# Performance work log

Hardware: AMD Instinct MI355X
Metric: run time of the kernel (lower is better)

## Reference

```python
import jax, jax.numpy as jnp
import numpy as np

NU, NI, ED, H = 30000, 10000, 64, 4
D = ED * H            # fusion_dim = 256
N = NU + NI           # total graph nodes
E = 100000            # edges
B = 8192              # scored (user, wine) pairs
NST, SD = 4, 64       # side tokens / side token dim
NEG = -1e30


def setup_inputs():
    key = jax.random.key(0)
    ks = iter(jax.random.split(key, 64))

    def w(*shape):
        return jax.random.normal(next(ks), shape, jnp.float32) * 0.05

    return {
        "user": jax.random.randint(next(ks), (B,), 0, NU),
        "wine": jax.random.randint(next(ks), (B,), 0, NI),
        "edge_index": jax.random.randint(next(ks), (2, E), 0, N),
        "keep_edge": jax.random.uniform(next(ks), (E,)) > 0.2,   # edge_dropout keep mask
        "node_mask": jax.random.uniform(next(ks), (N,)) < 0.2,   # mask-autoencoding mask
        "user_emb": w(NU, ED),
        "wine_emb": w(NI, ED),
        "up_w": w(ED, D), "up_b": w(D),
        "wp_w": w(ED, D), "wp_b": w(D),
        "sf_proj_w": w(SD, D), "sf_proj_b": w(D),
        "sf_q_w": w(D, D), "sf_q_b": w(D),
        "sf_k_w": w(D, D), "sf_k_b": w(D),
        "sf_v_w": w(D, D), "sf_v_b": w(D),
        "sf_o_w": w(D, D), "sf_o_b": w(D),
        "sf_fc_w": w(2 * D, D), "sf_fc_b": w(D),
        "g_w": w(D, D), "g_b": w(D),
        "t_q_w": w(D, H * D), "t_q_b": w(H * D),
        "t_k_w": w(D, H * D), "t_k_b": w(H * D),
        "t_v_w": w(D, H * D), "t_v_b": w(H * D),
        "t_skip_w": w(D, D), "t_skip_b": w(D),
        "fc_w": w(2 * D, 1), "fc_b": w(1),
        "ae_w": w(D, D), "ae_b": w(D),
        "ep_w": w(2 * D, 1), "ep_b": w(1),
        "wine_side_features": jax.random.normal(next(ks), (NI, NST, SD), jnp.float32),
    }


def _forward(user, wine, edge_index, keep_edge, node_mask,
             user_emb, wine_emb, up_w, up_b, wp_w, wp_b,
             sf_proj_w, sf_proj_b, sf_q_w, sf_q_b, sf_k_w, sf_k_b,
             sf_v_w, sf_v_b, sf_o_w, sf_o_b, sf_fc_w, sf_fc_b,
             g_w, g_b, t_q_w, t_q_b, t_k_w, t_k_b, t_v_w, t_v_b,
             t_skip_w, t_skip_b, fc_w, fc_b, ae_w, ae_b, ep_w, ep_b,
             wine_side_features):
    u_proj = user_emb @ up_w + up_b                       # [NU, D]
    w_proj = wine_emb @ wp_w + wp_b                       # [NI, D]

    # WineSideFusion: single-head attention of wine embedding over side tokens
    side = wine_side_features @ sf_proj_w + sf_proj_b     # [NI, T, D]
    q = w_proj @ sf_q_w + sf_q_b                          # [NI, D]
    k = side @ sf_k_w + sf_k_b                            # [NI, T, D]
    v = side @ sf_v_w + sf_v_b
    attn = jax.nn.softmax(jnp.einsum('nd,ntd->nt', q, k) / jnp.sqrt(jnp.float32(D)), axis=-1)
    ao = jnp.einsum('nt,ntd->nd', attn, v) @ sf_o_w + sf_o_b
    fused = jnp.concatenate([w_proj, ao], axis=1) @ sf_fc_w + sf_fc_b

    x = jnp.concatenate([u_proj, fused], axis=0)          # [N, D]
    src, dst = edge_index[0], edge_index[1]
    ew = keep_edge.astype(x.dtype)                        # edge dropout as 0/1 weights

    # GCNConv (add self loops, symmetric norm)
    deg = jax.ops.segment_sum(ew, dst, num_segments=N) + 1.0
    dinv = jax.lax.rsqrt(deg)
    norm = dinv[src] * dinv[dst] * ew                     # [E]
    xw = x @ g_w                                          # [N, D]
    agg = jax.ops.segment_sum(xw[src] * norm[:, None], dst, num_segments=N)
    x = agg + xw * (dinv * dinv)[:, None] + g_b

    # TransformerConv(heads=H, concat=False): mean over heads + skip
    qh = (x @ t_q_w + t_q_b).reshape(N, H, D)
    kh = (x @ t_k_w + t_k_b).reshape(N, H, D)
    vh = (x @ t_v_w + t_v_b).reshape(N, H, D)
    logits = jnp.einsum('ehd,ehd->eh', qh[dst], kh[src]) / jnp.sqrt(jnp.float32(D))
    logits = jnp.where(keep_edge[:, None], logits, NEG)
    m = jax.ops.segment_max(logits, dst, num_segments=N)  # [N, H]
    m = jnp.where(m < NEG / 2, 0.0, m)                    # guard empty segments
    e = jnp.exp(logits - m[dst]) * ew[:, None]            # [E, H]
    den = jax.ops.segment_sum(e, dst, num_segments=N)     # [N, H]
    num = jax.ops.segment_sum(e[:, :, None] * vh[src], dst, num_segments=N)  # [N, H, D]
    attn_out = num / jnp.maximum(den, 1e-16)[:, :, None]
    x = attn_out.mean(axis=1) + x @ t_skip_w + t_skip_b   # [N, D]

    # Masked autoencoding: masked rows are zeroed, then autoencoded -> recon = bias
    maskf = node_mask.astype(x.dtype)
    recon = ae_b                                          # 0 @ ae_w + ae_b
    diff = recon[None, :] - x                             # [N, D]
    recon_loss = jnp.sum(maskf[:, None] * diff * diff) / (jnp.sum(maskf) * D)

    u_out = x[user]                                       # [B, D]
    w_out = x[wine + NU]                                  # [B, D]
    pair = jnp.concatenate([u_out, w_out], axis=1)        # [B, 2D]

    edge_score = jax.nn.sigmoid(pair @ ep_w + ep_b)       # [B, 1]
    edge_pred_loss = jnp.mean((edge_score - 1.0) ** 2)

    score = jax.nn.sigmoid((pair @ fc_w + fc_b).squeeze(-1)) * 4.0 + 1.0  # [B]
    return score, recon_loss, edge_pred_loss


def reference(user, wine, edge_index, keep_edge, node_mask,
              user_emb, wine_emb, up_w, up_b, wp_w, wp_b,
              sf_proj_w, sf_proj_b, sf_q_w, sf_q_b, sf_k_w, sf_k_b,
              sf_v_w, sf_v_b, sf_o_w, sf_o_b, sf_fc_w, sf_fc_b,
              g_w, g_b, t_q_w, t_q_b, t_k_w, t_k_b, t_v_w, t_v_b,
              t_skip_w, t_skip_b, fc_w, fc_b, ae_w, ae_b, ep_w, ep_b,
              wine_side_features):
    return _forward(user, wine, edge_index, keep_edge, node_mask,
                    user_emb, wine_emb, up_w, up_b, wp_w, wp_b,
                    sf_proj_w, sf_proj_b, sf_q_w, sf_q_b, sf_k_w, sf_k_b,
                    sf_v_w, sf_v_b, sf_o_w, sf_o_b, sf_fc_w, sf_fc_b,
                    g_w, g_b, t_q_w, t_q_b, t_k_w, t_k_b, t_v_w, t_v_b,
                    t_skip_w, t_skip_b, fc_w, fc_b, ae_w, ae_b, ep_w, ep_b,
                    wine_side_features)
```

## Files before the change

### kernel.cpp

```cpp
#include <hip/hip_runtime.h>
#include <stdint.h>

typedef unsigned short u16;
typedef unsigned char u8;
typedef __attribute__((ext_vector_type(8))) short bf16x8;
typedef __attribute__((ext_vector_type(4))) float f32x4;

#define NU_C 30000
#define NI_C 10000
#define N_C  40000
#define E_C  100000
#define B_C  8192

static __device__ __forceinline__ float bf2f(u16 u) {
    union { unsigned int i; float f; } c; c.i = ((unsigned int)u) << 16; return c.f;
}
static __device__ __forceinline__ u16 f2bf(float f) {
    union { float f; unsigned int i; } c; c.f = f;
    return (u16)((c.i + 0x7FFFu + ((c.i >> 16) & 1u)) >> 16);
}
static __device__ __forceinline__ float wave_sum(float v) {
#pragma unroll
    for (int off = 32; off > 0; off >>= 1) v += __shfl_xor(v, off);
    return v;
}

__global__ void zero_kernel(unsigned int* p, int n) {
    int i = blockIdx.x * 256 + threadIdx.x;
    if (i < n) p[i] = 0u;
}
__global__ void fillval_kernel(float* p, int n, float v) {
    int i = blockIdx.x * 256 + threadIdx.x;
    if (i < n) p[i] = v;
}

__global__ void detect_kernel(const unsigned int* a, int n, int* flag) {
    int i = blockIdx.x * 256 + threadIdx.x;
    if (i >= n) return;
    unsigned int v = a[i];
    int f = 0;
    if (v > 1u) f |= 1;
    if (v != 0u && v != 0x3F800000u) f |= 2;
    if (f) atomicOr(flag, f);
}
__global__ void conv_masks_kernel(const void* keep_raw, const void* nm_raw,
                                  u8* km, u8* nm, int E, int N, const int* flag)
{
    int i = blockIdx.x * 256 + threadIdx.x;
    const int f = *flag;
    if (i < E) {
        u8 r;
        if ((f & 1) == 0)      r = ((const int*)keep_raw)[i] != 0;
        else if ((f & 2) == 0) r = ((const float*)keep_raw)[i] != 0.f;
        else                   r = ((const u8*)keep_raw)[i] != 0;
        km[i] = r;
    }
    int j = i - E;
    if (j >= 0 && j < N) {
        u8 r;
        if ((f & 1) == 0)      r = ((const int*)nm_raw)[j] != 0;
        else if ((f & 2) == 0) r = ((const float*)nm_raw)[j] != 0.f;
        else                   r = ((const u8*)nm_raw)[j] != 0;
        nm[j] = r;
    }
}

__global__ void conv3_kernel(const float* __restrict__ a, int na4,
                             const float* __restrict__ b, int nb4,
                             const float* __restrict__ c, int nc4,
                             u16* __restrict__ oa, u16* __restrict__ ob, u16* __restrict__ oc)
{
    int tot = na4 + nb4 + nc4;
    for (int i = blockIdx.x * 256 + threadIdx.x; i < tot; i += gridDim.x * 256) {
        const float* s; u16* o; int j = i;
        if (j < na4) { s = a; o = oa; }
        else if ((j -= na4) < nb4) { s = b; o = ob; }
        else { j -= nb4; s = c; o = oc; }
        float4 v = *(const float4*)&s[(size_t)j * 4];
        ushort4 r;
        r.x = f2bf(v.x); r.y = f2bf(v.y); r.z = f2bf(v.z); r.w = f2bf(v.w);
        *(ushort4*)&o[(size_t)j * 4] = r;
    }
}

#define WT_ELEMS 1359872
__device__ const int wd_prefix[23] = {0,16384,32768,49152,114688,180224,245760,311296,442368,
    507904,573440,638976,704512,770048,835584,901120,966656,1032192,1097728,1163264,1228800,
    1294336,1359872};
__device__ const u8  wd_src[22]  = {0,1,2,3,4,5,6,7,8,9,10,11,12,10,11,12,10,11,12,10,11,12};
__device__ const short wd_ldw[22]= {256,256,256,256,256,256,256,256,256,256,
    1024,1024,1024,1024,1024,1024,1024,1024,1024,1024,1024,1024};
__device__ const short wd_coff[22]={0,0,0,0,0,0,0,0,0,0, 0,0,0, 256,256,256, 512,512,512, 768,768,768};
__device__ const short wd_kmask[22]={63,63,63,255,255,255,255,511,255,255,
    255,255,255,255,255,255,255,255,255,255,255,255};
__device__ const u8  wd_ksh[22] = {6,6,6,8,8,8,8,9,8,8, 8,8,8,8,8,8,8,8,8,8,8,8};

__global__ __launch_bounds__(256)
void wtrans_kernel(const float* w0, const float* w1, const float* w2, const float* w3,
                   const float* w4, const float* w5, const float* w6, const float* w7,
                   const float* w8, const float* w9, const float* w10, const float* w11,
                   const float* w12, u16* __restrict__ WT)
{
    int idx = blockIdx.x * 256 + threadIdx.x;
    if (idx >= WT_ELEMS) return;
    int d = 0;
    while (wd_prefix[d + 1] <= idx) ++d;
    const int local = idx - wd_prefix[d];
    const int k = local & wd_kmask[d];
    const int n = local >> wd_ksh[d];
    const float* s;
    switch (wd_src[d]) {
        case 0: s = w0; break; case 1: s = w1; break; case 2: s = w2; break;
        case 3: s = w3; break; case 4: s = w4; break; case 5: s = w5; break;
        case 6: s = w6; break; case 7: s = w7; break; case 8: s = w8; break;
        case 9: s = w9; break; case 10: s = w10; break; case 11: s = w11; break;
        default: s = w12; break;
    }
    WT[idx] = f2bf(s[(size_t)k * wd_ldw[d] + wd_coff[d] + n]);
}

__global__ void prep_bias_kernel(const float* sfk_b, const float* sfv_b,
                                 const float* tq_b, const float* tk_b, const float* tv_b,
                                 float* kvb, float* qkvb)
{
    int i = blockIdx.x * 256 + threadIdx.x;
    if (i < 512) kvb[i] = i < 256 ? sfk_b[i] : sfv_b[i - 256];
    if (i < 3072) {
        int h = i / 768, j = i - h * 768;
        qkvb[i] = j < 256 ? tq_b[h * 256 + j]
                : (j < 512 ? tk_b[h * 256 + j - 256] : tv_b[h * 256 + j - 512]);
    }
}

template <typename OT>
__global__ __launch_bounds__(512)
void mgemm_kernel(const u16* __restrict__ A, int lda,
                  const u16* __restrict__ WT,
                  const float* __restrict__ bias,
                  OT* __restrict__ C, int ldc,
                  int M, int N, int K)
{
    __shared__ __align__(16) u16 As[256][72];
    __shared__ __align__(16) u16 Bs[128][72];
    const int t = threadIdx.x;
    const int wid = t >> 6, lane = t & 63;
    const int wr = wid >> 1, wc = wid & 1;
    const int lr = lane & 15, lg = lane >> 4;
    const int gx = gridDim.x;
    const int nwg = gx * gridDim.y;
    const int orig = blockIdx.y * gx + blockIdx.x;
    const int q8 = nwg >> 3, r8 = nwg & 7;
    const int xcd = orig & 7, oidx = orig >> 3;
    const int swzb = (xcd < r8 ? xcd * (q8 + 1) : r8 * (q8 + 1) + (xcd - r8) * q8) + oidx;
    const int row0 = (swzb / gx) * 256, col0 = (swzb % gx) * 128;
    const int sra = t >> 1, sha = (t & 1) * 32;
    const int srb = t >> 2, shb = (t & 3) * 16;
    f32x4 acc[4][4] = {};

    for (int k0 = 0; k0 < K; k0 += 64) {
        {
            const int gr = row0 + sra;
            if (gr < M) {
                const u16* ap = &A[(size_t)gr * lda + k0 + sha];
#pragma unroll
                for (int j = 0; j < 4; ++j)
                    *(bf16x8*)&As[sra][sha + j * 8] = *(const bf16x8*)&ap[j * 8];
            } else {
                const bf16x8 z = {0, 0, 0, 0, 0, 0, 0, 0};
#pragma unroll
                for (int j = 0; j < 4; ++j)
                    *(bf16x8*)&As[sra][sha + j * 8] = z;
            }
        }
        {
            const u16* bp = &WT[(size_t)(col0 + srb) * K + k0 + shb];
#pragma unroll
            for (int j = 0; j < 2; ++j)
                *(bf16x8*)&Bs[srb][shb + j * 8] = *(const bf16x8*)&bp[j * 8];
        }
        __syncthreads();
#pragma unroll
        for (int kk = 0; kk < 2; ++kk) {
            bf16x8 af[4], bfr[4];
#pragma unroll
            for (int m = 0; m < 4; ++m)
                af[m] = *(const bf16x8*)&As[wr * 64 + m * 16 + lr][kk * 32 + lg * 8];
#pragma unroll
            for (int n = 0; n < 4; ++n)
                bfr[n] = *(const bf16x8*)&Bs[wc * 64 + n * 16 + lr][kk * 32 + lg * 8];
#pragma unroll
            for (int m = 0; m < 4; ++m)
#pragma unroll
                for (int n = 0; n < 4; ++n)
                    acc[m][n] = __builtin_amdgcn_mfma_f32_16x16x32_bf16(af[m], bfr[n], acc[m][n], 0, 0, 0);
        }
        __syncthreads();
    }
#pragma unroll
    for (int m = 0; m < 4; ++m) {
#pragma unroll
        for (int r = 0; r < 4; ++r) {
            int row = row0 + wr * 64 + m * 16 + lg * 4 + r;
            if (row >= M) continue;
#pragma unroll
            for (int n = 0; n < 4; ++n) {
                int col = col0 + wc * 64 + n * 16 + lr;
                float v = acc[m][n][r];
                if (bias) v += bias[col];
                if constexpr (sizeof(OT) == 4) C[(size_t)row * ldc + col] = v;
                else C[(size_t)row * ldc + col] = f2bf(v);
            }
        }
    }
}

__global__ __launch_bounds__(256)
void side_attn_kernel(const u16* __restrict__ q, const u16* __restrict__ kv,
                      u16* __restrict__ ao, int NI)
{
    const int wid = threadIdx.x >> 6, lane = threadIdx.x & 63;
    const int n = blockIdx.x * 4 + wid;
    if (n >= NI) return;
    const ushort4 qu = *(const ushort4*)&q[(size_t)n * 256 + lane * 4];
    const float q0 = bf2f(qu.x), q1 = bf2f(qu.y), q2 = bf2f(qu.z), q3 = bf2f(qu.w);
    float logit[4];
#pragma unroll
    for (int tk = 0; tk < 4; ++tk) {
        const ushort4 ku = *(const ushort4*)&kv[((size_t)n * 4 + tk) * 512 + lane * 4];
        float p = q0 * bf2f(ku.x) + q1 * bf2f(ku.y) + q2 * bf2f(ku.z) + q3 * bf2f(ku.w);
        logit[tk] = wave_sum(p) * (1.f / 16.f);
    }
    float mx = fmaxf(fmaxf(logit[0], logit[1]), fmaxf(logit[2], logit[3]));
    float e[4], den = 0.f;
#pragma unroll
    for (int tk = 0; tk < 4; ++tk) { e[tk] = __expf(logit[tk] - mx); den += e[tk]; }
    const float inv = 1.f / den;
    float o0 = 0.f, o1 = 0.f, o2 = 0.f, o3 = 0.f;
#pragma unroll
    for (int tk = 0; tk < 4; ++tk) {
        const ushort4 vu = *(const ushort4*)&kv[((size_t)n * 4 + tk) * 512 + 256 + lane * 4];
        const float w = e[tk] * inv;
        o0 = fmaf(w, bf2f(vu.x), o0); o1 = fmaf(w, bf2f(vu.y), o1);
        o2 = fmaf(w, bf2f(vu.z), o2); o3 = fmaf(w, bf2f(vu.w), o3);
    }
    ushort4 o;
    o.x = f2bf(o0); o.y = f2bf(o1); o.z = f2bf(o2); o.w = f2bf(o3);
    *(ushort4*)&ao[(size_t)n * 256 + lane * 4] = o;
}

__global__ void count_kernel(const int* __restrict__ dst, const u8* __restrict__ keep,
                             int* __restrict__ cnt, float* __restrict__ degw, int E)
{
    int e = blockIdx.x * 256 + threadIdx.x;
    if (e >= E) return;
    int d = dst[e];
    atomicAdd(&cnt[d], 1);
    if (keep[e]) atomicAdd(&degw[d], 1.f);
}

__global__ void dinv_kernel(const float* __restrict__ degw, float* __restrict__ dinv, int N)
{
    int n = blockIdx.x * 256 + threadIdx.x;
    if (n < N) dinv[n] = rsqrtf(degw[n] + 1.f);
}

__global__ __launch_bounds__(1024)
void scan_kernel(const int* __restrict__ cnt, int* __restrict__ rs, int n)
{
    __shared__ int wsum[17];
    __shared__ int s_run;
    const int t = threadIdx.x, lane = t & 63, wid = t >> 6;
    if (t == 0) s_run = 0;
    __syncthreads();
    for (int base = 0; base < n; base += 1024) {
        int i = base + t;
        int v = (i < n) ? cnt[i] : 0;
        int x = v;
#pragma unroll
        for (int off = 1; off < 64; off <<= 1) {
            int y = __shfl_up(x, off);
            if (lane >= off) x += y;
        }
        if (lane == 63) wsum[wid] = x;
        __syncthreads();
        if (t == 0) {
            int a = 0;
            for (int j = 0; j < 16; ++j) { int tmp = wsum[j]; wsum[j] = a; a += tmp; }
            wsum[16] = a;
        }
        __syncthreads();
        if (i < n) rs[i] = s_run + wsum[wid] + x - v;
        __syncthreads();
        if (t == 0) s_run += wsum[16];
        __syncthreads();
    }
    if (t == 0) rs[n] = s_run;
}

__global__ void fill_kernel(const int* __restrict__ dst, const int* __restrict__ rs,
                            int* __restrict__ cursor, int* __restrict__ eid, int E)
{
    int e = blockIdx.x * 256 + threadIdx.x;
    if (e >= E) return;
    int d = dst[e];
    int p = atomicAdd(&cursor[d], 1);
    eid[rs[d] + p] = e;
}

__global__ void sort_kernel(const int* __restrict__ rs, int* __restrict__ eid, int N)
{
    int n = blockIdx.x * 256 + threadIdx.x;
    if (n >= N) return;
    const int b = rs[n], len = rs[n + 1] - b;
    for (int i = 1; i < len; ++i) {
        int key = eid[b + i];
        int j = i - 1;
        while (j >= 0 && eid[b + j] > key) { eid[b + j + 1] = eid[b + j]; --j; }
        eid[b + j + 1] = key;
    }
}

__global__ void edge_prep_kernel(const int* __restrict__ eid, const int* __restrict__ src,
                                 const int* __restrict__ dst, const u8* __restrict__ keep,
                                 const float* __restrict__ dinv,
                                 int* __restrict__ ssrc, float* __restrict__ wnorm, int E)
{
    int i = blockIdx.x * 256 + threadIdx.x;
    if (i >= E) return;
    const int e = eid[i];
    const int s = src[e];
    const u8 k = keep[e];
    ssrc[i] = s * 2 + (int)k;
    wnorm[i] = k ? dinv[s] * dinv[dst[e]] : 0.f;
}

__global__ __launch_bounds__(256)
void gcn_kernel(const u16* __restrict__ xw, const int* __restrict__ ssrc,
                const float* __restrict__ wnorm, const int* __restrict__ rs,
                const float* __restrict__ dinv, const float* __restrict__ gb,
                u16* __restrict__ xout, int N)
{
    const int wid = threadIdx.x >> 6, lane = threadIdx.x & 63;
    const int n = blockIdx.x * 4 + wid;
    if (n >= N) return;
    const float di = dinv[n];
    const float dii = di * di;
    const ushort4 own = *(const ushort4*)&xw[(size_t)n * 256 + lane * 4];
    float a0 = bf2f(own.x) * dii, a1 = bf2f(own.y) * dii;
    float a2 = bf2f(own.z) * dii, a3 = bf2f(own.w) * dii;
    const int e0 = rs[n], e1 = rs[n + 1];
    for (int i = e0; i < e1; ++i) {
        const float w = wnorm[i];
        const int s = ssrc[i] >> 1;
        const ushort4 r = *(const ushort4*)&xw[(size_t)s * 256 + lane * 4];
        a0 = fmaf(bf2f(r.x), w, a0); a1 = fmaf(bf2f(r.y), w, a1);
        a2 = fmaf(bf2f(r.z), w, a2); a3 = fmaf(bf2f(r.w), w, a3);
    }
    const float4 g = *(const float4*)&gb[lane * 4];
    ushort4 o;
    o.x = f2bf(a0 + g.x); o.y = f2bf(a1 + g.y);
    o.z = f2bf(a2 + g.z); o.w = f2bf(a3 + g.w);
    *(ushort4*)&xout[(size_t)n * 256 + lane * 4] = o;
}

__global__ __launch_bounds__(256)
void tconv_head_kernel(const u16* __restrict__ qkv, const int* __restrict__ ssrc,
                       const int* __restrict__ rs, float* __restrict__ xacc, int N)
{
    const int wid = threadIdx.x >> 6, lane = threadIdx.x & 63;
    const int n = blockIdx.x * 4 + wid;
    if (n >= N) return;
    const ushort4 qu = *(const ushort4*)&qkv[(size_t)n * 768 + lane * 4];
    const float q0 = bf2f(qu.x), q1 = bf2f(qu.y), q2 = bf2f(qu.z), q3 = bf2f(qu.w);
    const int e0 = rs[n], e1 = rs[n + 1];
    float m = -1e30f, den = 0.f;
    float a0 = 0.f, a1 = 0.f, a2 = 0.f, a3 = 0.f;
    int i = e0;
    for (; i + 1 < e1; i += 2) {
        const int va = ssrc[i], vb = ssrc[i + 1];
        const int sa = va >> 1, sb = vb >> 1;
        const float ewa = (float)(va & 1), ewb = (float)(vb & 1);
        const ushort4 ka = *(const ushort4*)&qkv[(size_t)sa * 768 + 256 + lane * 4];
        const ushort4 kb = *(const ushort4*)&qkv[(size_t)sb * 768 + 256 + lane * 4];
        const ushort4 xa = *(const ushort4*)&qkv[(size_t)sa * 768 + 512 + lane * 4];
        const ushort4 xb4 = *(const ushort4*)&qkv[(size_t)sb * 768 + 512 + lane * 4];
        float pa = q0 * bf2f(ka.x) + q1 * bf2f(ka.y) + q2 * bf2f(ka.z) + q3 * bf2f(ka.w);
        float pb = q0 * bf2f(kb.x) + q1 * bf2f(kb.y) + q2 * bf2f(kb.z) + q3 * bf2f(kb.w);
        pa = wave_sum(pa) * (1.f / 16.f);
        pb = wave_sum(pb) * (1.f / 16.f);
        {
            const float mn = fmaxf(m, pa);
            const float sc = __expf(m - mn);
            const float w = __expf(pa - mn) * ewa;
            den = den * sc + w;
            a0 = fmaf(w, bf2f(xa.x), a0 * sc); a1 = fmaf(w, bf2f(xa.y), a1 * sc);
            a2 = fmaf(w, bf2f(xa.z), a2 * sc); a3 = fmaf(w, bf2f(xa.w), a3 * sc);
            m = mn;
        }
        {
            const float mn = fmaxf(m, pb);
            const float sc = __expf(m - mn);
            const float w = __expf(pb - mn) * ewb;
            den = den * sc + w;
            a0 = fmaf(w, bf2f(xb4.x), a0 * sc); a1 = fmaf(w, bf2f(xb4.y), a1 * sc);
            a2 = fmaf(w, bf2f(xb4.z), a2 * sc); a3 = fmaf(w, bf2f(xb4.w), a3 * sc);
            m = mn;
        }
    }
    if (i < e1) {
        const int va = ssrc[i];
        const int sa = va >> 1;
        const float ewa = (float)(va & 1);
        const ushort4 ka = *(const ushort4*)&qkv[(size_t)sa * 768 + 256 + lane * 4];
        const ushort4 xa = *(const ushort4*)&qkv[(size_t)sa * 768 + 512 + lane * 4];
        float pa = q0 * bf2f(ka.x) + q1 * bf2f(ka.y) + q2 * bf2f(ka.z) + q3 * bf2f(ka.w);
        pa = wave_sum(pa) * (1.f / 16.f);
        const float mn = fmaxf(m, pa);
        const float sc = __expf(m - mn);
        const float w = __expf(pa - mn) * ewa;
        den = den * sc + w;
        a0 = fmaf(w, bf2f(xa.x), a0 * sc); a1 = fmaf(w, bf2f(xa.y), a1 * sc);
        a2 = fmaf(w, bf2f(xa.z), a2 * sc); a3 = fmaf(w, bf2f(xa.w), a3 * sc);
    }
    const float inv = 0.25f / fmaxf(den, 1e-16f);
    float4* p4 = (float4*)&xacc[(size_t)n * 256 + lane * 4];
    float4 cur = *p4;
    cur.x += a0 * inv; cur.y += a1 * inv; cur.z += a2 * inv; cur.w += a3 * inv;
    *p4 = cur;
}

__global__ __launch_bounds__(256)
void recon_kernel(const float* __restrict__ x, const u8* __restrict__ mask,
                  const float* __restrict__ aeb,
                  float* __restrict__ rblkS, float* __restrict__ rblkC, int N)
{
    const int total = N * 256;
    float s = 0.f, c = 0.f;
    for (int idx = blockIdx.x * 256 + threadIdx.x; idx < total; idx += gridDim.x * 256) {
        const int n = idx >> 8, d = idx & 255;
        if (mask[n]) {
            const float diff = aeb[d] - x[idx];
            s = fmaf(diff, diff, s);
            if (d == 0) c += 1.f;
        }
    }
    s = wave_sum(s); c = wave_sum(c);
    __shared__ float ss[4], cc[4];
    const int lane = threadIdx.x & 63, wid = threadIdx.x >> 6;
    if (lane == 0) { ss[wid] = s; cc[wid] = c; }
    __syncthreads();
    if (threadIdx.x == 0) {
        rblkS[blockIdx.x] = ss[0] + ss[1] + ss[2] + ss[3];
        rblkC[blockIdx.x] = cc[0] + cc[1] + cc[2] + cc[3];
    }
}

__global__ __launch_bounds__(256)
void score_kernel(const float* __restrict__ x, const int* __restrict__ user,
                  const int* __restrict__ wine,
                  const float* __restrict__ epw, const float* __restrict__ epb,
                  const float* __restrict__ fcw, const float* __restrict__ fcb,
                  float* __restrict__ out, float* __restrict__ sblk, int B)
{
    __shared__ float sep[4];
    const int wid = threadIdx.x >> 6, lane = threadIdx.x & 63;
    const int b = blockIdx.x * 4 + wid;
    if (b < B) {
        const size_t u = (size_t)user[b];
        const size_t w = (size_t)wine[b] + NU_C;
        const float4 xu = *(const float4*)&x[u * 256 + lane * 4];
        const float4 xw = *(const float4*)&x[w * 256 + lane * 4];
        const float4 e1 = *(const float4*)&epw[lane * 4];
        const float4 e2 = *(const float4*)&epw[256 + lane * 4];
        const float4 f1 = *(const float4*)&fcw[lane * 4];
        const float4 f2 = *(const float4*)&fcw[256 + lane * 4];
        float pep = xu.x * e1.x + xu.y * e1.y + xu.z * e1.z + xu.w * e1.w
                  + xw.x * e2.x + xw.y * e2.y + xw.z * e2.z + xw.w * e2.w;
        float pfc = xu.x * f1.x + xu.y * f1.y + xu.z * f1.z + xu.w * f1.w
                  + xw.x * f2.x + xw.y * f2.y + xw.z * f2.z + xw.w * f2.w;
        pep = wave_sum(pep); pfc = wave_sum(pfc);
        if (lane == 0) {
            const float es = 1.f / (1.f + __expf(-(pep + epb[0])));
            sep[wid] = (es - 1.f) * (es - 1.f);
            out[b] = 1.f / (1.f + __expf(-(pfc + fcb[0]))) * 4.f + 1.f;
        }
    } else if (lane == 0) {
        sep[wid] = 0.f;
    }
    __syncthreads();
    if (threadIdx.x == 0) sblk[blockIdx.x] = sep[0] + sep[1] + sep[2] + sep[3];
}

__global__ __launch_bounds__(1024)
void final_reduce_kernel(const float* __restrict__ rblkS, const float* __restrict__ rblkC,
                         const float* __restrict__ sblk, float* __restrict__ out, int B)
{
    const int t = threadIdx.x, lane = t & 63, wid = t >> 6;
    float s = rblkS[t] + rblkS[t + 1024];
    float c = rblkC[t] + rblkC[t + 1024];
    float p = sblk[t] + sblk[t + 1024];
    s = wave_sum(s); c = wave_sum(c); p = wave_sum(p);
    __shared__ float ss[16], cc[16], pp[16];
    if (lane == 0) { ss[wid] = s; cc[wid] = c; pp[wid] = p; }
    __syncthreads();
    if (t == 0) {
        float S = 0.f, C = 0.f, P = 0.f;
        for (int i = 0; i < 16; ++i) { S += ss[i]; C += cc[i]; P += pp[i]; }
        out[B] = S / (C * 256.f);
        out[B + 1] = P / (float)B;
    }
}

extern "C" void kernel_launch(void* const* d_in, const int* in_sizes, int n_in,
                              void* d_out, int out_size, void* d_ws, size_t ws_size,
                              hipStream_t stream)
{
    const int* user = (const int*)d_in[0];
    const int* wine = (const int*)d_in[1];
    const int* e_src = (const int*)d_in[2];
    const int* e_dst = e_src + E_C;
    const void* keep_raw  = d_in[3];
    const void* nmask_raw = d_in[4];
    const float* user_emb = (const float*)d_in[5];
    const float* wine_emb = (const float*)d_in[6];
    const float* up_w = (const float*)d_in[7];
    const float* up_b = (const float*)d_in[8];
    const float* wp_w = (const float*)d_in[9];
    const float* wp_b = (const float*)d_in[10];
    const float* sf_proj_w = (const float*)d_in[11];
    const float* sf_proj_b = (const float*)d_in[12];
    const float* sf_q_w = (const float*)d_in[13];
    const float* sf_q_b = (const float*)d_in[14];
    const float* sf_k_w = (const float*)d_in[15];
    const float* sf_k_b = (const float*)d_in[16];
    const float* sf_v_w = (const float*)d_in[17];
    const float* sf_v_b = (const float*)d_in[18];
    const float* sf_o_w = (const float*)d_in[19];
    const float* sf_o_b = (const float*)d_in[20];
    const float* sf_fc_w = (const float*)d_in[21];
    const float* sf_fc_b = (const float*)d_in[22];
    const float* g_w = (const float*)d_in[23];
    const float* g_b = (const float*)d_in[24];
    const float* t_q_w = (const float*)d_in[25];
    const float* t_q_b = (const float*)d_in[26];
    const float* t_k_w = (const float*)d_in[27];
    const float* t_k_b = (const float*)d_in[28];
    const float* t_v_w = (const float*)d_in[29];
    const float* t_v_b = (const float*)d_in[30];
    const float* t_skip_w = (const float*)d_in[31];
    const float* t_skip_b = (const float*)d_in[32];
    const float* fc_w = (const float*)d_in[33];
    const float* fc_b = (const float*)d_in[34];
    const float* ae_b = (const float*)d_in[36];
    const float* ep_w = (const float*)d_in[37];
    const float* ep_b = (const float*)d_in[38];
    const float* wsf = (const float*)d_in[39];
    float* out = (float*)d_out;
    char* ws = (char*)d_ws;

    size_t off = 0;
    auto take = [&](size_t b) { size_t r = off; off += (b + 255) & ~(size_t)255; return r; };
    const size_t o_xb     = take((size_t)N_C * 256 * 2);
    const size_t o_cnt    = take((size_t)N_C * 4);
    const size_t o_degw   = take((size_t)N_C * 4);
    const size_t o_cursor = take((size_t)N_C * 4);
    const size_t o_scal   = take(256);
    const size_t o_rowst  = take((size_t)(N_C + 1) * 4);
    const size_t o_dinv   = take((size_t)N_C * 4);
    const size_t o_eid    = take((size_t)E_C * 4);
    const size_t o_ssrc   = take((size_t)E_C * 4);
    const size_t o_wnorm  = take((size_t)E_C * 4);
    const size_t o_kmask  = take((size_t)E_C);
    const size_t o_nmask  = take((size_t)N_C);
    const size_t o_rblkS  = take(2048 * 4);
    const size_t o_rblkC  = take(2048 * 4);
    const size_t o_sblk   = take(2048 * 4);
    const size_t o_wt     = take((size_t)WT_ELEMS * 2);
    const size_t o_bias   = take(3584 * 4);
    const size_t ARENA    = 102400000;
    const size_t o_arena  = take(ARENA);
    const size_t NEED = off;

    if (ws_size < NEED) {
        fillval_kernel<<<dim3((out_size + 255) / 256), 256, 0, stream>>>(
            out, out_size, (float)((double)ws_size / (1024.0 * 1024.0)));
        return;
    }

    u16*   xb     = (u16*)  (ws + o_xb);
    int*   cnt    = (int*)  (ws + o_cnt);
    float* degw   = (float*)(ws + o_degw);
    int*   cursor = (int*)  (ws + o_cursor);
    int*   flag   = (int*)  (ws + o_scal);
    int*   rowst  = (int*)  (ws + o_rowst);
    float* dinvb  = (float*)(ws + o_dinv);
    int*   eid    = (int*)  (ws + o_eid);
    int*   ssrc   = (int*)  (ws + o_ssrc);
    float* wnorm  = (float*)(ws + o_wnorm);
    u8*    kmask  = (u8*)   (ws + o_kmask);
    u8*    nmaskb = (u8*)   (ws + o_nmask);
    float* rblkS  = (float*)(ws + o_rblkS);
    float* rblkC  = (float*)(ws + o_rblkC);
    float* sblk   = (float*)(ws + o_sblk);
    u16*   WT     = (u16*)  (ws + o_wt);
    float* kvb    = (float*)(ws + o_bias);
    float* qkvb   = kvb + 512;

    u16* wt_up   = WT + 0;
    u16* wt_wp   = WT + 16384;
    u16* wt_proj = WT + 32768;
    u16* wt_sfq  = WT + 49152;
    u16* wt_sfkv = WT + 114688;
    u16* wt_sfo  = WT + 245760;
    u16* wt_sffc = WT + 311296;
    u16* wt_g    = WT + 442368;
    u16* wt_skip = WT + 507904;
    u16* wt_qkv  = WT + 573440;

    u16* ue16  = (u16*)(ws + o_arena);
    u16* we16  = (u16*)(ws + o_arena + 3840000);
    u16* wsf16 = (u16*)(ws + o_arena + 5120000);
    u16* cat   = (u16*)(ws + o_arena + 10240000);
    u16* side  = (u16*)(ws + o_arena + 20480000);
    u16* qbuf  = (u16*)(ws + o_arena + 40960000);
    u16* kvbuf = (u16*)(ws + o_arena + 46080000);
    u16* aobuf = (u16*)(ws + o_arena + 87040000);
    u16* xw    = (u16*)(ws + o_arena);
    u16* qkvh  = (u16*)(ws + o_arena);
    float* xacc = (float*)(ws + o_arena + 61440000);

    const int zero_words = (3 * N_C * 4 + 256) / 4;
    zero_kernel<<<dim3((zero_words + 255) / 256), 256, 0, stream>>>((unsigned int*)cnt, zero_words);

    detect_kernel<<<dim3((E_C / 4 + 255) / 256), 256, 0, stream>>>((const unsigned int*)keep_raw, E_C / 4, flag);
    conv_masks_kernel<<<dim3((E_C + N_C + 255) / 256), 256, 0, stream>>>(keep_raw, nmask_raw, kmask, nmaskb, E_C, N_C, flag);

    conv3_kernel<<<dim3(2048), 256, 0, stream>>>(user_emb, NU_C * 16, wine_emb, NI_C * 16,
                                                 wsf, N_C * 16, ue16, we16, wsf16);
    wtrans_kernel<<<dim3(WT_ELEMS / 256), 256, 0, stream>>>(up_w, wp_w, sf_proj_w, sf_q_w,
        sf_k_w, sf_v_w, sf_o_w, sf_fc_w, g_w, t_skip_w, t_q_w, t_k_w, t_v_w, WT);
    prep_bias_kernel<<<dim3(12), 256, 0, stream>>>(sf_k_b, sf_v_b, t_q_b, t_k_b, t_v_b, kvb, qkvb);

    mgemm_kernel<u16><<<dim3(2, 118), 512, 0, stream>>>(ue16, 64, wt_up, up_b, xb, 256, NU_C, 256, 64);
    mgemm_kernel<u16><<<dim3(2, 40), 512, 0, stream>>>(we16, 64, wt_wp, wp_b, cat, 512, NI_C, 256, 64);
    mgemm_kernel<u16><<<dim3(2, 157), 512, 0, stream>>>(wsf16, 64, wt_proj, sf_proj_b, side, 256, N_C, 256, 64);
    mgemm_kernel<u16><<<dim3(2, 40), 512, 0, stream>>>(cat, 512, wt_sfq, sf_q_b, qbuf, 256, NI_C, 256, 256);
    mgemm_kernel<u16><<<dim3(4, 157), 512, 0, stream>>>(side, 256, wt_sfkv, kvb, kvbuf, 512, N_C, 512, 256);
    side_attn_kernel<<<dim3(2500), 256, 0, stream>>>(qbuf, kvbuf, aobuf, NI_C);
    mgemm_kernel<u16><<<dim3(2, 40), 512, 0, stream>>>(aobuf, 256, wt_sfo, sf_o_b, cat + 256, 512, NI_C, 256, 256);
    mgemm_kernel<u16><<<dim3(2, 40), 512, 0, stream>>>(cat, 512, wt_sffc, sf_fc_b, xb + (size_t)NU_C * 256, 256, NI_C, 256, 512);

    count_kernel<<<dim3((E_C + 255) / 256), 256, 0, stream>>>(e_dst, kmask, cnt, degw, E_C);
    dinv_kernel<<<dim3((N_C + 255) / 256), 256, 0, stream>>>(degw, dinvb, N_C);
    scan_kernel<<<dim3(1), 1024, 0, stream>>>(cnt, rowst, N_C);
    fill_kernel<<<dim3((E_C + 255) / 256), 256, 0, stream>>>(e_dst, rowst, cursor, eid, E_C);
    sort_kernel<<<dim3((N_C + 255) / 256), 256, 0, stream>>>(rowst, eid, N_C);
    edge_prep_kernel<<<dim3((E_C + 255) / 256), 256, 0, stream>>>(eid, e_src, e_dst, kmask, dinvb, ssrc, wnorm, E_C);

    mgemm_kernel<u16><<<dim3(2, 157), 512, 0, stream>>>(xb, 256, wt_g, nullptr, xw, 256, N_C, 256, 256);
    gcn_kernel<<<dim3(N_C / 4), 256, 0, stream>>>(xw, ssrc, wnorm, rowst, dinvb, g_b, xb, N_C);

    mgemm_kernel<float><<<dim3(2, 157), 512, 0, stream>>>(xb, 256, wt_skip, t_skip_b, xacc, 256, N_C, 256, 256);
    for (int h = 0; h < 4; ++h) {
        mgemm_kernel<u16><<<dim3(6, 157), 512, 0, stream>>>(xb, 256, wt_qkv + h * 196608,
                                                            qkvb + h * 768, qkvh, 768, N_C, 768, 256);
        tconv_head_kernel<<<dim3(N_C / 4), 256, 0, stream>>>(qkvh, ssrc, rowst, xacc, N_C);
    }

    recon_kernel<<<dim3(2048), 256, 0, stream>>>(xacc, nmaskb, ae_b, rblkS, rblkC, N_C);
    score_kernel<<<dim3(2048), 256, 0, stream>>>(xacc, user, wine, ep_w, ep_b, fc_w, fc_b, out, sblk, B_C);
    final_reduce_kernel<<<dim3(1), 1024, 0, stream>>>(rblkS, rblkC, sblk, out, B_C);
}
```

Measured before the change: 615.8 us.

## Widen GEMM tile to 256x256 with 16 waves and dynamic shared memory

The bf16 MFMA GEMM goes from 256x128 tiles with 8 waves to 256x256 tiles with 16 waves (1024 threads). Shared memory moves to a 72 KB dynamic allocation, and the grid x-dimension is halved at every launch. The A tile no longer branches per row for bounds: the row index is clamped and a select writes zeros. Each A tile is now reused across twice as many output columns, but blocks get fewer and larger, which cuts the number of workgroups (e.g. 157 for N=256) and can hurt occupancy on a 256-CU part.

Result: slower. 630.6 us (+2.4%).

```diff
diff --git a/kernel.cpp b/kernel.cpp
--- a/kernel.cpp
+++ b/kernel.cpp
@@ -133,18 +133,19 @@
 }
 
 template <typename OT>
-__global__ __launch_bounds__(512)
+__global__ __launch_bounds__(1024)
 void mgemm_kernel(const u16* __restrict__ A, int lda,
                   const u16* __restrict__ WT,
                   const float* __restrict__ bias,
                   OT* __restrict__ C, int ldc,
                   int M, int N, int K)
 {
-    __shared__ __align__(16) u16 As[256][72];
-    __shared__ __align__(16) u16 Bs[128][72];
+    extern __shared__ __align__(16) u16 smem[];
+    u16 (*As)[72] = (u16(*)[72])smem;
+    u16 (*Bs)[72] = (u16(*)[72])(smem + 256 * 72);
     const int t = threadIdx.x;
     const int wid = t >> 6, lane = t & 63;
-    const int wr = wid >> 1, wc = wid & 1;
+    const int wr = wid >> 2, wc = wid & 3;
     const int lr = lane & 15, lg = lane >> 4;
     const int gx = gridDim.x;
     const int nwg = gx * gridDim.y;
@@ -152,32 +153,21 @@
     const int q8 = nwg >> 3, r8 = nwg & 7;
     const int xcd = orig & 7, oidx = orig >> 3;
     const int swzb = (xcd < r8 ? xcd * (q8 + 1) : r8 * (q8 + 1) + (xcd - r8) * q8) + oidx;
-    const int row0 = (swzb / gx) * 256, col0 = (swzb % gx) * 128;
-    const int sra = t >> 1, sha = (t & 1) * 32;
-    const int srb = t >> 2, shb = (t & 3) * 16;
+    const int row0 = (swzb / gx) * 256, col0 = (swzb % gx) * 256;
+    const int sr = t >> 2, sh = (t & 3) * 16;
+    const bool avalid = (row0 + sr) < M;
+    const u16* aptr = &A[(size_t)min(row0 + sr, M - 1) * lda];
+    const u16* bptr = &WT[(size_t)(col0 + sr) * K];
+    const bf16x8 z = {0, 0, 0, 0, 0, 0, 0, 0};
     f32x4 acc[4][4] = {};
 
     for (int k0 = 0; k0 < K; k0 += 64) {
-        {
-            const int gr = row0 + sra;
-            if (gr < M) {
-                const u16* ap = &A[(size_t)gr * lda + k0 + sha];
-#pragma unroll
-                for (int j = 0; j < 4; ++j)
-                    *(bf16x8*)&As[sra][sha + j * 8] = *(const bf16x8*)&ap[j * 8];
-            } else {
-                const bf16x8 z = {0, 0, 0, 0, 0, 0, 0, 0};
-#pragma unroll
-                for (int j = 0; j < 4; ++j)
-                    *(bf16x8*)&As[sra][sha + j * 8] = z;
-            }
-        }
-        {
-            const u16* bp = &WT[(size_t)(col0 + srb) * K + k0 + shb];
-#pragma unroll
-            for (int j = 0; j < 2; ++j)
-                *(bf16x8*)&Bs[srb][shb + j * 8] = *(const bf16x8*)&bp[j * 8];
-        }
+#pragma unroll
+        for (int j = 0; j < 2; ++j)
+            *(bf16x8*)&As[sr][sh + j * 8] = avalid ? *(const bf16x8*)&aptr[k0 + sh + j * 8] : z;
+#pragma unroll
+        for (int j = 0; j < 2; ++j)
+            *(bf16x8*)&Bs[sr][sh + j * 8] = *(const bf16x8*)&bptr[k0 + sh + j * 8];
         __syncthreads();
 #pragma unroll
         for (int kk = 0; kk < 2; ++kk) {
@@ -629,6 +619,8 @@
     u16* qkvh  = (u16*)(ws + o_arena);
     float* xacc = (float*)(ws + o_arena + 61440000);
 
+    const int SMEM = 73728;
+
     const int zero_words = (3 * N_C * 4 + 256) / 4;
     zero_kernel<<<dim3((zero_words + 255) / 256), 256, 0, stream>>>((unsigned int*)cnt, zero_words);
 
@@ -641,14 +633,14 @@
         sf_k_w, sf_v_w, sf_o_w, sf_fc_w, g_w, t_skip_w, t_q_w, t_k_w, t_v_w, WT);
     prep_bias_kernel<<<dim3(12), 256, 0, stream>>>(sf_k_b, sf_v_b, t_q_b, t_k_b, t_v_b, kvb, qkvb);
 
-    mgemm_kernel<u16><<<dim3(2, 118), 512, 0, stream>>>(ue16, 64, wt_up, up_b, xb, 256, NU_C, 256, 64);
-    mgemm_kernel<u16><<<dim3(2, 40), 512, 0, stream>>>(we16, 64, wt_wp, wp_b, cat, 512, NI_C, 256, 64);
-    mgemm_kernel<u16><<<dim3(2, 157), 512, 0, stream>>>(wsf16, 64, wt_proj, sf_proj_b, side, 256, N_C, 256, 64);
-    mgemm_kernel<u16><<<dim3(2, 40), 512, 0, stream>>>(cat, 512, wt_sfq, sf_q_b, qbuf, 256, NI_C, 256, 256);
-    mgemm_kernel<u16><<<dim3(4, 157), 512, 0, stream>>>(side, 256, wt_sfkv, kvb, kvbuf, 512, N_C, 512, 256);
+    mgemm_kernel<u16><<<dim3(1, 118), 1024, SMEM, stream>>>(ue16, 64, wt_up, up_b, xb, 256, NU_C, 256, 64);
+    mgemm_kernel<u16><<<dim3(1, 40), 1024, SMEM, stream>>>(we16, 64, wt_wp, wp_b, cat, 512, NI_C, 256, 64);
+    mgemm_kernel<u16><<<dim3(1, 157), 1024, SMEM, stream>>>(wsf16, 64, wt_proj, sf_proj_b, side, 256, N_C, 256, 64);
+    mgemm_kernel<u16><<<dim3(1, 40), 1024, SMEM, stream>>>(cat, 512, wt_sfq, sf_q_b, qbuf, 256, NI_C, 256, 256);
+    mgemm_kernel<u16><<<dim3(2, 157), 1024, SMEM, stream>>>(side, 256, wt_sfkv, kvb, kvbuf, 512, N_C, 512, 256);
     side_attn_kernel<<<dim3(2500), 256, 0, stream>>>(qbuf, kvbuf, aobuf, NI_C);
-    mgemm_kernel<u16><<<dim3(2, 40), 512, 0, stream>>>(aobuf, 256, wt_sfo, sf_o_b, cat + 256, 512, NI_C, 256, 256);
-    mgemm_kernel<u16><<<dim3(2, 40), 512, 0, stream>>>(cat, 512, wt_sffc, sf_fc_b, xb + (size_t)NU_C * 256, 256, NI_C, 256, 512);
+    mgemm_kernel<u16><<<dim3(1, 40), 1024, SMEM, stream>>>(aobuf, 256, wt_sfo, sf_o_b, cat + 256, 512, NI_C, 256, 256);
+    mgemm_kernel<u16><<<dim3(1, 40), 1024, SMEM, stream>>>(cat, 512, wt_sffc, sf_fc_b, xb + (size_t)NU_C * 256, 256, NI_C, 256, 512);
 
     count_kernel<<<dim3((E_C + 255) / 256), 256, 0, stream>>>(e_dst, kmask, cnt, degw, E_C);
     dinv_kernel<<<dim3((N_C + 255) / 256), 256, 0, stream>>>(degw, dinvb, N_C);
@@ -657,13 +649,13 @@
     sort_kernel<<<dim3((N_C + 255) / 256), 256, 0, stream>>>(rowst, eid, N_C);
     edge_prep_kernel<<<dim3((E_C + 255) / 256), 256, 0, stream>>>(eid, e_src, e_dst, kmask, dinvb, ssrc, wnorm, E_C);
 
-    mgemm_kernel<u16><<<dim3(2, 157), 512, 0, stream>>>(xb, 256, wt_g, nullptr, xw, 256, N_C, 256, 256);
+    mgemm_kernel<u16><<<dim3(1, 157), 1024, SMEM, stream>>>(xb, 256, wt_g, nullptr, xw, 256, N_C, 256, 256);
     gcn_kernel<<<dim3(N_C / 4), 256, 0, stream>>>(xw, ssrc, wnorm, rowst, dinvb, g_b, xb, N_C);
 
-    mgemm_kernel<float><<<dim3(2, 157), 512, 0, stream>>>(xb, 256, wt_skip, t_skip_b, xacc, 256, N_C, 256, 256);
+    mgemm_kernel<float><<<dim3(1, 157), 1024, SMEM, stream>>>(xb, 256, wt_skip, t_skip_b, xacc, 256, N_C, 256, 256);
     for (int h = 0; h < 4; ++h) {
-        mgemm_kernel<u16><<<dim3(6, 157), 512, 0, stream>>>(xb, 256, wt_qkv + h * 196608,
-                                                            qkvb + h * 768, qkvh, 768, N_C, 768, 256);
+        mgemm_kernel<u16><<<dim3(3, 157), 1024, SMEM, stream>>>(xb, 256, wt_qkv + h * 196608,
+                                                                qkvb + h * 768, qkvh, 768, N_C, 768, 256);
         tconv_head_kernel<<<dim3(N_C / 4), 256, 0, stream>>>(qkvh, ssrc, rowst, xacc, N_C);
     }
 
```
